# Kernel optimization log

Hardware: AMD Instinct MI355X
Metric: run time of the kernel (lower is better)

## Reference

```python
import jax, jax.numpy as jnp
import numpy as np

N_NODES = 50000
N_EDGES = 1600000
D_IN = 256
N_HEADS = 4
D_OUT = 32
NEG_SLOPE = 0.2


def setup_inputs() -> dict:
    key = jax.random.key(0)
    ks = jax.random.split(key, 7)
    return {
        "feat": jax.random.normal(ks[0], (N_NODES, D_IN), dtype=jnp.float32),
        "fc_w": jax.random.normal(ks[1], (N_HEADS * D_OUT, D_IN), dtype=jnp.float32) * 0.05,
        "attn_l": jax.random.normal(ks[2], (1, N_HEADS, D_OUT), dtype=jnp.float32) * 0.1,
        "attn_r": jax.random.normal(ks[3], (1, N_HEADS, D_OUT), dtype=jnp.float32) * 0.1,
        "bias": jax.random.normal(ks[4], (N_HEADS * D_OUT,), dtype=jnp.float32) * 0.01,
        "src": jax.random.randint(ks[5], (N_EDGES,), 0, N_NODES, dtype=jnp.int32),
        "dst": jax.random.randint(ks[6], (N_EDGES,), 0, N_NODES, dtype=jnp.int32),
    }


def reference(feat, fc_w, attn_l, attn_r, bias, src, dst):
    N = feat.shape[0]
    H, D = attn_l.shape[1], attn_l.shape[2]
    # projected features: [N, H, D] (torch Linear: x @ W.T)
    h = (feat @ fc_w.T).reshape(N, H, D)
    # per-node attention logits: [N, H]
    el = (h * attn_l).sum(-1)
    er = (h * attn_r).sum(-1)
    # per-edge score with leaky relu: [E, H]
    e = el[src] + er[dst]
    e = jnp.where(e > 0, e, NEG_SLOPE * e)
    # edge softmax normalized over incoming edges of each dst node
    m = jax.ops.segment_max(e, dst, num_segments=N)
    m = jnp.where(jnp.isfinite(m), m, 0.0)  # nodes with no in-edges
    ex = jnp.exp(e - m[dst])
    denom = jax.ops.segment_sum(ex, dst, num_segments=N)
    a = ex / jnp.maximum(denom[dst], 1e-9)  # [E, H]
    # weighted scatter-aggregate: [N, H, D]
    msg = h[src] * a[:, :, None]
    out = jax.ops.segment_sum(msg, dst, num_segments=N)
    out = out + bias.reshape(1, H, D)
    return out
```

## Files before the change

### kernel.cpp

```cpp
#include <hip/hip_runtime.h>
#include <hip/hip_bf16.h>
#include <math.h>

#define D_IN   256
#define HD     128
#define NHEAD  4
#define NEG_SLOPE 0.2f
#define CHUNK 32
#define MAXB  1024
#define BCAP  2560

typedef _Float16 h8 __attribute__((ext_vector_type(8)));
typedef _Float16 h4 __attribute__((ext_vector_type(4)));
typedef _Float16 h2 __attribute__((ext_vector_type(2)));
typedef float f4 __attribute__((ext_vector_type(4)));

#define SWZ(row, byte) ((byte) ^ (((row) & 7) << 4))

__global__ void zero_k(int* __restrict__ gcur, int B) {
    int i = blockIdx.x * 256 + threadIdx.x;
    if (i < B) gcur[i] = 0;
}

__global__ __launch_bounds__(256) void bin_k(const int* __restrict__ src,
                                             const int* __restrict__ dst,
                                             int* __restrict__ gcur,
                                             unsigned int* __restrict__ pairs,
                                             int E, int B) {
    __shared__ int lcnt[MAXB];
    __shared__ int lbase[MAXB];
    const int t = threadIdx.x;
    for (int i = t; i < B; i += 256) lcnt[i] = 0;
    __syncthreads();
    const int base = blockIdx.x * 4096;
    int sv[16], dv[16];
    #pragma unroll
    for (int k = 0; k < 16; ++k) {
        int idx = base + k * 256 + t;
        if (idx < E) {
            sv[k] = src[idx];
            dv[k] = dst[idx];
            atomicAdd(&lcnt[dv[k] >> 6], 1);
        } else dv[k] = -1;
    }
    __syncthreads();
    for (int i = t; i < B; i += 256) {
        int c = lcnt[i];
        lbase[i] = c ? atomicAdd(&gcur[i], c) : 0;
        lcnt[i] = 0;
    }
    __syncthreads();
    #pragma unroll
    for (int k = 0; k < 16; ++k) {
        if (dv[k] >= 0) {
            int b = dv[k] >> 6;
            int r = lbase[b] + atomicAdd(&lcnt[b], 1);
            if (r < BCAP)
                pairs[(size_t)b * BCAP + r] = ((unsigned int)sv[k] << 6) | (unsigned int)(dv[k] & 63);
        }
    }
}

__global__ __launch_bounds__(256) void bucket_k(const unsigned int* __restrict__ pairs,
                                                const int* __restrict__ gcur,
                                                int* __restrict__ row_start,
                                                int* __restrict__ degs,
                                                int* __restrict__ srcs, int N) {
    __shared__ int cnt64[64];
    __shared__ int base64[64];
    const int b = blockIdx.x;
    const int t = threadIdx.x;
    const int lo = b * BCAP;
    const int len = min(gcur[b], BCAP);
    if (t < 64) cnt64[t] = 0;
    __syncthreads();
    for (int i = t; i < len; i += 256)
        atomicAdd(&cnt64[pairs[lo + i] & 63], 1);
    __syncthreads();
    if (t < 64) {
        int v = cnt64[t];
        int x = v;
        #pragma unroll
        for (int o = 1; o < 64; o <<= 1) {
            int y = __shfl_up(x, o);
            if (t >= o) x += y;
        }
        int excl = lo + x - v;
        base64[t] = excl;
        int d = b * 64 + t;
        if (d < N) { row_start[d] = excl; degs[d] = v; }
        cnt64[t] = 0;
    }
    __syncthreads();
    for (int i = lo + t; i < lo + len; i += 256) {
        unsigned int p = pairs[i];
        int ld = p & 63;
        int r = atomicAdd(&cnt64[ld], 1);
        srcs[base64[ld] + r] = (int)(p >> 6);
    }
}

__global__ __launch_bounds__(256) void gemm_k(
        const float* __restrict__ feat, const float* __restrict__ fcw,
        const float* __restrict__ attn_l, const float* __restrict__ attn_r,
        unsigned int* __restrict__ hbuf, float* __restrict__ el, float* __restrict__ er,
        int N) {
    __shared__ __align__(16) unsigned char lds_raw[64 * 512];
    const int t  = threadIdx.x;
    const int l  = t & 63;
    const int w  = t >> 6;
    const int l4 = l >> 4;
    const int lm = l & 15;
    const int n0 = blockIdx.x * 64;

    h8 breg[2][8];
    #pragma unroll
    for (int jt = 0; jt < 2; ++jt) {
        const float* wrow = fcw + (size_t)(w * 32 + jt * 16 + lm) * D_IN;
        #pragma unroll
        for (int ks = 0; ks < 8; ++ks) {
            int k = ks * 32 + l4 * 8;
            float4 a = *(const float4*)&wrow[k];
            float4 b = *(const float4*)&wrow[k + 4];
            h8 p = {(_Float16)a.x, (_Float16)a.y, (_Float16)a.z, (_Float16)a.w,
                    (_Float16)b.x, (_Float16)b.y, (_Float16)b.z, (_Float16)b.w};
            breg[jt][ks] = p;
        }
    }

    #pragma unroll
    for (int i = 0; i < 16; ++i) {
        int idx = t + 256 * i;
        int row = idx >> 6, c4 = idx & 63;
        float4 v = make_float4(0.f, 0.f, 0.f, 0.f);
        if (n0 + row < N) v = *(const float4*)&feat[(size_t)(n0 + row) * D_IN + c4 * 4];
        h4 p = {(_Float16)v.x, (_Float16)v.y, (_Float16)v.z, (_Float16)v.w};
        *(h4*)(lds_raw + row * 512 + SWZ(row, c4 * 8)) = p;
    }
    __syncthreads();

    f4 acc[4][2] = {};
    #pragma unroll
    for (int ks = 0; ks < 8; ++ks) {
        #pragma unroll
        for (int mt = 0; mt < 4; ++mt) {
            int row = mt * 16 + lm;
            h8 af = *(const h8*)(lds_raw + row * 512 + SWZ(row, (ks * 32 + l4 * 8) * 2));
            acc[mt][0] = __builtin_amdgcn_mfma_f32_16x16x32_f16(af, breg[0][ks], acc[mt][0], 0, 0, 0);
            acc[mt][1] = __builtin_amdgcn_mfma_f32_16x16x32_f16(af, breg[1][ks], acc[mt][1], 0, 0, 0);
        }
    }

    float al[2], ar[2];
    #pragma unroll
    for (int jt = 0; jt < 2; ++jt) {
        al[jt] = attn_l[w * 32 + jt * 16 + lm];
        ar[jt] = attn_r[w * 32 + jt * 16 + lm];
    }
    #pragma unroll
    for (int mt = 0; mt < 4; ++mt) {
        #pragma unroll
        for (int r = 0; r < 4; ++r) {
            float vl = acc[mt][0][r] * al[0] + acc[mt][1][r] * al[1];
            float vr = acc[mt][0][r] * ar[0] + acc[mt][1][r] * ar[1];
            #pragma unroll
            for (int o = 1; o < 16; o <<= 1) {
                vl += __shfl_xor(vl, o);
                vr += __shfl_xor(vr, o);
            }
            int node = n0 + mt * 16 + l4 * 4 + r;
            if (lm == 0 && node < N) {
                el[node * NHEAD + w] = vl;
                er[node * NHEAD + w] = vr;
            }
        }
    }

    __syncthreads();
    unsigned short* hl = (unsigned short*)lds_raw;
    #pragma unroll
    for (int mt = 0; mt < 4; ++mt)
        #pragma unroll
        for (int jt = 0; jt < 2; ++jt)
            #pragma unroll
            for (int r = 0; r < 4; ++r) {
                int node_local = mt * 16 + l4 * 4 + r;
                int ch = w * 32 + jt * 16 + lm;
                _Float16 hf = (_Float16)acc[mt][jt][r];
                hl[node_local * 128 + ch] = __builtin_bit_cast(unsigned short, hf);
            }
    __syncthreads();
    const unsigned int* hu = (const unsigned int*)lds_raw;
    #pragma unroll
    for (int i = 0; i < 16; ++i) {
        int idx = t + 256 * i;
        int row = idx >> 6, c = idx & 63;
        if (n0 + row < N) hbuf[(size_t)(n0 + row) * 64 + c] = hu[row * 64 + c];
    }
}

__global__ __launch_bounds__(64) void agg_k(
        const int* __restrict__ row_start, const int* __restrict__ degs,
        const int* __restrict__ srcs,
        const float* __restrict__ el, const float* __restrict__ er,
        const unsigned int* __restrict__ hbuf, const float* __restrict__ bias,
        float* __restrict__ out, int N) {
    __shared__ float exw[CHUNK * NHEAD];
    __shared__ int s_lds[CHUNK];
    const int d = blockIdx.x;
    const int l = threadIdx.x;
    const int he = l >> 4, es = l & 15;
    const int half = l >> 5, cl = l & 31;
    const int hc = cl >> 3;
    const int base = row_start[d];
    const int deg  = degs[d];
    const float erd = er[d * NHEAD + he];

    f4 acc = {0.f, 0.f, 0.f, 0.f};
    float den = 0.f;

    for (int c0 = 0; c0 < deg; c0 += CHUNK) {
        const int clen = min(CHUNK, deg - c0);
        __syncthreads();
        int s0 = -1, s1 = -1;
        if (es < clen)      s0 = srcs[base + c0 + es];
        if (es + 16 < clen) s1 = srcs[base + c0 + es + 16];
        float e0 = 0.f, e1 = 0.f;
        if (s0 >= 0) e0 = el[s0 * NHEAD + he];
        if (s1 >= 0) e1 = el[s1 * NHEAD + he];
        if (s0 >= 0) {
            float v = e0 + erd;
            v = v > 0.f ? v : NEG_SLOPE * v;
            float ex = __expf(v);
            if (he == 0) s_lds[es] = s0;
            exw[es * NHEAD + he] = ex;
            den += ex;
        }
        if (s1 >= 0) {
            float v = e1 + erd;
            v = v > 0.f ? v : NEG_SLOPE * v;
            float ex = __expf(v);
            if (he == 0) s_lds[es + 16] = s1;
            exw[(es + 16) * NHEAD + he] = ex;
            den += ex;
        }
        __syncthreads();
        for (int jj = 0; jj < clen; jj += 8) {
            uint2 hv[4];
            float ex4[4];
            int e2v[4];
            #pragma unroll
            for (int k = 0; k < 4; ++k) {
                int e2 = jj + 2 * k + half;
                e2v[k] = (e2 < clen) ? e2 : -1;
                if (e2v[k] >= 0) {
                    int s = s_lds[e2];
                    hv[k] = *(const uint2*)&hbuf[(size_t)s * 64 + cl * 2];
                    ex4[k] = exw[e2 * NHEAD + hc];
                }
            }
            #pragma unroll
            for (int k = 0; k < 4; ++k) {
                if (e2v[k] >= 0) {
                    h2 p0 = __builtin_bit_cast(h2, hv[k].x);
                    h2 p1 = __builtin_bit_cast(h2, hv[k].y);
                    acc[0] += (float)p0[0] * ex4[k];
                    acc[1] += (float)p0[1] * ex4[k];
                    acc[2] += (float)p1[0] * ex4[k];
                    acc[3] += (float)p1[1] * ex4[k];
                }
            }
        }
    }

    #pragma unroll
    for (int k = 0; k < 4; ++k) acc[k] += __shfl_xor(acc[k], 32);
    #pragma unroll
    for (int o = 1; o < 16; o <<= 1) den += __shfl_xor(den, o);
    float denc = __shfl(den, hc << 4);
    float r = 1.0f / fmaxf(denc, 1e-9f);

    if (half == 0) {
        float4 b4 = *(const float4*)&bias[cl * 4];
        float4 o4 = make_float4(acc[0] * r + b4.x, acc[1] * r + b4.y,
                                acc[2] * r + b4.z, acc[3] * r + b4.w);
        *(float4*)&out[(size_t)d * HD + cl * 4] = o4;
    }
}

extern "C" void kernel_launch(void* const* d_in, const int* in_sizes, int n_in,
                              void* d_out, int out_size, void* d_ws, size_t ws_size,
                              hipStream_t stream) {
    const float* feat   = (const float*)d_in[0];
    const float* fcw    = (const float*)d_in[1];
    const float* attn_l = (const float*)d_in[2];
    const float* attn_r = (const float*)d_in[3];
    const float* bias   = (const float*)d_in[4];
    const int*   src    = (const int*)d_in[5];
    const int*   dst    = (const int*)d_in[6];
    float* out = (float*)d_out;

    const int N = in_sizes[0] / D_IN;
    const int E = in_sizes[5];
    const int B = (N + 63) >> 6;

    unsigned int* hbuf = (unsigned int*)d_ws;
    float* el        = (float*)(hbuf + (size_t)N * 64);
    float* er        = el + (size_t)N * NHEAD;
    unsigned int* pairs = (unsigned int*)(er + (size_t)N * NHEAD);
    int*   srcs      = (int*)(pairs + (size_t)B * BCAP);
    int*   row_start = srcs + (size_t)B * BCAP;
    int*   degs      = row_start + N;
    int*   gcur      = degs + N;

    const int ebl = (E + 4095) / 4096;

    zero_k<<<(B + 255) / 256, 256, 0, stream>>>(gcur, B);
    bin_k<<<ebl, 256, 0, stream>>>(src, dst, gcur, pairs, E, B);
    bucket_k<<<B, 256, 0, stream>>>(pairs, gcur, row_start, degs, srcs, N);
    gemm_k<<<(N + 63) / 64, 256, 0, stream>>>(feat, fcw, attn_l, attn_r, hbuf, el, er, N);
    agg_k<<<N, 64, 0, stream>>>(row_start, degs, srcs, el, er, hbuf, bias, out, N);
}
```

Measured before the change: 137.9 us.

## Fuse GEMM with edge binning and restructure aggregation to wave-per-node

Merges the edge binning kernel and the projection GEMM into one launch, with block index selecting the role, so the two independent phases run concurrently. The zeroing kernel is replaced by a memset. The aggregation kernel now maps one wavefront per destination node, four nodes per block. It broadcasts source indices and exp weights through shuffles instead of LDS and barriers, and loads 16-byte feature vectors per lane. This removes per-node launch granularity and syncthreads overhead but adds shuffle work and extra cross-lane reductions.

```diff
diff --git a/kernel.cpp b/kernel.cpp
--- a/kernel.cpp
+++ b/kernel.cpp
@@ -6,7 +6,6 @@
 #define HD     128
 #define NHEAD  4
 #define NEG_SLOPE 0.2f
-#define CHUNK 32
 #define MAXB  1024
 #define BCAP  2560
 
@@ -17,47 +16,141 @@
 
 #define SWZ(row, byte) ((byte) ^ (((row) & 7) << 4))
 
-__global__ void zero_k(int* __restrict__ gcur, int B) {
-    int i = blockIdx.x * 256 + threadIdx.x;
-    if (i < B) gcur[i] = 0;
-}
-
-__global__ __launch_bounds__(256) void bin_k(const int* __restrict__ src,
-                                             const int* __restrict__ dst,
-                                             int* __restrict__ gcur,
-                                             unsigned int* __restrict__ pairs,
-                                             int E, int B) {
-    __shared__ int lcnt[MAXB];
-    __shared__ int lbase[MAXB];
+__global__ __launch_bounds__(256) void fused_k(
+        const float* __restrict__ feat, const float* __restrict__ fcw,
+        const float* __restrict__ attn_l, const float* __restrict__ attn_r,
+        unsigned int* __restrict__ hbuf, float* __restrict__ el, float* __restrict__ er,
+        const int* __restrict__ src, const int* __restrict__ dst,
+        int* __restrict__ gcur, unsigned int* __restrict__ pairs,
+        int N, int E, int B, int GB) {
+    __shared__ __align__(16) unsigned char smem[64 * 512];
     const int t = threadIdx.x;
-    for (int i = t; i < B; i += 256) lcnt[i] = 0;
-    __syncthreads();
-    const int base = blockIdx.x * 4096;
-    int sv[16], dv[16];
-    #pragma unroll
-    for (int k = 0; k < 16; ++k) {
-        int idx = base + k * 256 + t;
-        if (idx < E) {
-            sv[k] = src[idx];
-            dv[k] = dst[idx];
-            atomicAdd(&lcnt[dv[k] >> 6], 1);
-        } else dv[k] = -1;
-    }
-    __syncthreads();
-    for (int i = t; i < B; i += 256) {
-        int c = lcnt[i];
-        lbase[i] = c ? atomicAdd(&gcur[i], c) : 0;
-        lcnt[i] = 0;
-    }
-    __syncthreads();
-    #pragma unroll
-    for (int k = 0; k < 16; ++k) {
-        if (dv[k] >= 0) {
-            int b = dv[k] >> 6;
-            int r = lbase[b] + atomicAdd(&lcnt[b], 1);
-            if (r < BCAP)
-                pairs[(size_t)b * BCAP + r] = ((unsigned int)sv[k] << 6) | (unsigned int)(dv[k] & 63);
-        }
+
+    if ((int)blockIdx.x >= GB) {
+        int* lcnt  = (int*)smem;
+        int* lbase = lcnt + MAXB;
+        for (int i = t; i < B; i += 256) lcnt[i] = 0;
+        __syncthreads();
+        const int base = ((int)blockIdx.x - GB) * 4096;
+        int sv[16], dv[16];
+        #pragma unroll
+        for (int k = 0; k < 16; ++k) {
+            int idx = base + k * 256 + t;
+            if (idx < E) {
+                sv[k] = src[idx];
+                dv[k] = dst[idx];
+                atomicAdd(&lcnt[dv[k] >> 6], 1);
+            } else dv[k] = -1;
+        }
+        __syncthreads();
+        for (int i = t; i < B; i += 256) {
+            int c = lcnt[i];
+            lbase[i] = c ? atomicAdd(&gcur[i], c) : 0;
+            lcnt[i] = 0;
+        }
+        __syncthreads();
+        #pragma unroll
+        for (int k = 0; k < 16; ++k) {
+            if (dv[k] >= 0) {
+                int b = dv[k] >> 6;
+                int r = lbase[b] + atomicAdd(&lcnt[b], 1);
+                if (r < BCAP)
+                    pairs[(size_t)b * BCAP + r] = ((unsigned int)sv[k] << 6) | (unsigned int)(dv[k] & 63);
+            }
+        }
+        return;
+    }
+
+    unsigned char* lds_raw = smem;
+    const int l  = t & 63;
+    const int w  = t >> 6;
+    const int l4 = l >> 4;
+    const int lm = l & 15;
+    const int n0 = blockIdx.x * 64;
+
+    h8 breg[2][8];
+    #pragma unroll
+    for (int jt = 0; jt < 2; ++jt) {
+        const float* wrow = fcw + (size_t)(w * 32 + jt * 16 + lm) * D_IN;
+        #pragma unroll
+        for (int ks = 0; ks < 8; ++ks) {
+            int k = ks * 32 + l4 * 8;
+            float4 a = *(const float4*)&wrow[k];
+            float4 b = *(const float4*)&wrow[k + 4];
+            h8 p = {(_Float16)a.x, (_Float16)a.y, (_Float16)a.z, (_Float16)a.w,
+                    (_Float16)b.x, (_Float16)b.y, (_Float16)b.z, (_Float16)b.w};
+            breg[jt][ks] = p;
+        }
+    }
+
+    #pragma unroll
+    for (int i = 0; i < 16; ++i) {
+        int idx = t + 256 * i;
+        int row = idx >> 6, c4 = idx & 63;
+        float4 v = make_float4(0.f, 0.f, 0.f, 0.f);
+        if (n0 + row < N) v = *(const float4*)&feat[(size_t)(n0 + row) * D_IN + c4 * 4];
+        h4 p = {(_Float16)v.x, (_Float16)v.y, (_Float16)v.z, (_Float16)v.w};
+        *(h4*)(lds_raw + row * 512 + SWZ(row, c4 * 8)) = p;
+    }
+    __syncthreads();
+
+    f4 acc[4][2] = {};
+    #pragma unroll
+    for (int ks = 0; ks < 8; ++ks) {
+        #pragma unroll
+        for (int mt = 0; mt < 4; ++mt) {
+            int row = mt * 16 + lm;
+            h8 af = *(const h8*)(lds_raw + row * 512 + SWZ(row, (ks * 32 + l4 * 8) * 2));
+            acc[mt][0] = __builtin_amdgcn_mfma_f32_16x16x32_f16(af, breg[0][ks], acc[mt][0], 0, 0, 0);
+            acc[mt][1] = __builtin_amdgcn_mfma_f32_16x16x32_f16(af, breg[1][ks], acc[mt][1], 0, 0, 0);
+        }
+    }
+
+    float al[2], ar[2];
+    #pragma unroll
+    for (int jt = 0; jt < 2; ++jt) {
+        al[jt] = attn_l[w * 32 + jt * 16 + lm];
+        ar[jt] = attn_r[w * 32 + jt * 16 + lm];
+    }
+    #pragma unroll
+    for (int mt = 0; mt < 4; ++mt) {
+        #pragma unroll
+        for (int r = 0; r < 4; ++r) {
+            float vl = acc[mt][0][r] * al[0] + acc[mt][1][r] * al[1];
+            float vr = acc[mt][0][r] * ar[0] + acc[mt][1][r] * ar[1];
+            #pragma unroll
+            for (int o = 1; o < 16; o <<= 1) {
+                vl += __shfl_xor(vl, o);
+                vr += __shfl_xor(vr, o);
+            }
+            int node = n0 + mt * 16 + l4 * 4 + r;
+            if (lm == 0 && node < N) {
+                el[node * NHEAD + w] = vl;
+                er[node * NHEAD + w] = vr;
+            }
+        }
+    }
+
+    __syncthreads();
+    unsigned short* hl = (unsigned short*)lds_raw;
+    #pragma unroll
+    for (int mt = 0; mt < 4; ++mt)
+        #pragma unroll
+        for (int jt = 0; jt < 2; ++jt)
+            #pragma unroll
+            for (int r = 0; r < 4; ++r) {
+                int node_local = mt * 16 + l4 * 4 + r;
+                int ch = w * 32 + jt * 16 + lm;
+                _Float16 hf = (_Float16)acc[mt][jt][r];
+                hl[node_local * 128 + ch] = __builtin_bit_cast(unsigned short, hf);
+            }
+    __syncthreads();
+    const unsigned int* hu = (const unsigned int*)lds_raw;
+    #pragma unroll
+    for (int i = 0; i < 16; ++i) {
+        int idx = t + 256 * i;
+        int row = idx >> 6, c = idx & 63;
+        if (n0 + row < N) hbuf[(size_t)(n0 + row) * 64 + c] = hu[row * 64 + c];
     }
 }
 
@@ -100,191 +193,90 @@
     }
 }
 
-__global__ __launch_bounds__(256) void gemm_k(
-        const float* __restrict__ feat, const float* __restrict__ fcw,
-        const float* __restrict__ attn_l, const float* __restrict__ attn_r,
-        unsigned int* __restrict__ hbuf, float* __restrict__ el, float* __restrict__ er,
-        int N) {
-    __shared__ __align__(16) unsigned char lds_raw[64 * 512];
-    const int t  = threadIdx.x;
-    const int l  = t & 63;
-    const int w  = t >> 6;
-    const int l4 = l >> 4;
-    const int lm = l & 15;
-    const int n0 = blockIdx.x * 64;
-
-    h8 breg[2][8];
-    #pragma unroll
-    for (int jt = 0; jt < 2; ++jt) {
-        const float* wrow = fcw + (size_t)(w * 32 + jt * 16 + lm) * D_IN;
-        #pragma unroll
-        for (int ks = 0; ks < 8; ++ks) {
-            int k = ks * 32 + l4 * 8;
-            float4 a = *(const float4*)&wrow[k];
-            float4 b = *(const float4*)&wrow[k + 4];
-            h8 p = {(_Float16)a.x, (_Float16)a.y, (_Float16)a.z, (_Float16)a.w,
-                    (_Float16)b.x, (_Float16)b.y, (_Float16)b.z, (_Float16)b.w};
-            breg[jt][ks] = p;
-        }
-    }
-
-    #pragma unroll
-    for (int i = 0; i < 16; ++i) {
-        int idx = t + 256 * i;
-        int row = idx >> 6, c4 = idx & 63;
-        float4 v = make_float4(0.f, 0.f, 0.f, 0.f);
-        if (n0 + row < N) v = *(const float4*)&feat[(size_t)(n0 + row) * D_IN + c4 * 4];
-        h4 p = {(_Float16)v.x, (_Float16)v.y, (_Float16)v.z, (_Float16)v.w};
-        *(h4*)(lds_raw + row * 512 + SWZ(row, c4 * 8)) = p;
-    }
-    __syncthreads();
-
-    f4 acc[4][2] = {};
-    #pragma unroll
-    for (int ks = 0; ks < 8; ++ks) {
-        #pragma unroll
-        for (int mt = 0; mt < 4; ++mt) {
-            int row = mt * 16 + lm;
-            h8 af = *(const h8*)(lds_raw + row * 512 + SWZ(row, (ks * 32 + l4 * 8) * 2));
-            acc[mt][0] = __builtin_amdgcn_mfma_f32_16x16x32_f16(af, breg[0][ks], acc[mt][0], 0, 0, 0);
-            acc[mt][1] = __builtin_amdgcn_mfma_f32_16x16x32_f16(af, breg[1][ks], acc[mt][1], 0, 0, 0);
-        }
-    }
-
-    float al[2], ar[2];
-    #pragma unroll
-    for (int jt = 0; jt < 2; ++jt) {
-        al[jt] = attn_l[w * 32 + jt * 16 + lm];
-        ar[jt] = attn_r[w * 32 + jt * 16 + lm];
-    }
-    #pragma unroll
-    for (int mt = 0; mt < 4; ++mt) {
-        #pragma unroll
-        for (int r = 0; r < 4; ++r) {
-            float vl = acc[mt][0][r] * al[0] + acc[mt][1][r] * al[1];
-            float vr = acc[mt][0][r] * ar[0] + acc[mt][1][r] * ar[1];
-            #pragma unroll
-            for (int o = 1; o < 16; o <<= 1) {
-                vl += __shfl_xor(vl, o);
-                vr += __shfl_xor(vr, o);
-            }
-            int node = n0 + mt * 16 + l4 * 4 + r;
-            if (lm == 0 && node < N) {
-                el[node * NHEAD + w] = vl;
-                er[node * NHEAD + w] = vr;
-            }
-        }
-    }
-
-    __syncthreads();
-    unsigned short* hl = (unsigned short*)lds_raw;
-    #pragma unroll
-    for (int mt = 0; mt < 4; ++mt)
-        #pragma unroll
-        for (int jt = 0; jt < 2; ++jt)
-            #pragma unroll
-            for (int r = 0; r < 4; ++r) {
-                int node_local = mt * 16 + l4 * 4 + r;
-                int ch = w * 32 + jt * 16 + lm;
-                _Float16 hf = (_Float16)acc[mt][jt][r];
-                hl[node_local * 128 + ch] = __builtin_bit_cast(unsigned short, hf);
-            }
-    __syncthreads();
-    const unsigned int* hu = (const unsigned int*)lds_raw;
-    #pragma unroll
-    for (int i = 0; i < 16; ++i) {
-        int idx = t + 256 * i;
-        int row = idx >> 6, c = idx & 63;
-        if (n0 + row < N) hbuf[(size_t)(n0 + row) * 64 + c] = hu[row * 64 + c];
-    }
-}
-
-__global__ __launch_bounds__(64) void agg_k(
+__global__ __launch_bounds__(256) void agg_k(
         const int* __restrict__ row_start, const int* __restrict__ degs,
         const int* __restrict__ srcs,
         const float* __restrict__ el, const float* __restrict__ er,
         const unsigned int* __restrict__ hbuf, const float* __restrict__ bias,
         float* __restrict__ out, int N) {
-    __shared__ float exw[CHUNK * NHEAD];
-    __shared__ int s_lds[CHUNK];
-    const int d = blockIdx.x;
-    const int l = threadIdx.x;
-    const int he = l >> 4, es = l & 15;
-    const int half = l >> 5, cl = l & 31;
-    const int hc = cl >> 3;
+    const int l = threadIdx.x & 63;
+    const int d = blockIdx.x * 4 + (threadIdx.x >> 6);
+    if (d >= N) return;
+    const int q  = l >> 4;
+    const int es = l & 15;
+    const int hc = es >> 2;
     const int base = row_start[d];
     const int deg  = degs[d];
-    const float erd = er[d * NHEAD + he];
-
-    f4 acc = {0.f, 0.f, 0.f, 0.f};
+    const float erd = er[d * NHEAD + q];
+
+    float acc[8] = {0.f, 0.f, 0.f, 0.f, 0.f, 0.f, 0.f, 0.f};
     float den = 0.f;
 
-    for (int c0 = 0; c0 < deg; c0 += CHUNK) {
-        const int clen = min(CHUNK, deg - c0);
-        __syncthreads();
-        int s0 = -1, s1 = -1;
-        if (es < clen)      s0 = srcs[base + c0 + es];
-        if (es + 16 < clen) s1 = srcs[base + c0 + es + 16];
-        float e0 = 0.f, e1 = 0.f;
-        if (s0 >= 0) e0 = el[s0 * NHEAD + he];
-        if (s1 >= 0) e1 = el[s1 * NHEAD + he];
-        if (s0 >= 0) {
-            float v = e0 + erd;
+    for (int c0 = 0; c0 < deg; c0 += 32) {
+        const int clen = min(32, deg - c0);
+        int s0 = 0, s1 = 0;
+        float ex0 = 0.f, ex1 = 0.f;
+        if (es < clen) {
+            s0 = srcs[base + c0 + es];
+            float v = el[s0 * NHEAD + q] + erd;
             v = v > 0.f ? v : NEG_SLOPE * v;
-            float ex = __expf(v);
-            if (he == 0) s_lds[es] = s0;
-            exw[es * NHEAD + he] = ex;
-            den += ex;
-        }
-        if (s1 >= 0) {
-            float v = e1 + erd;
+            ex0 = __expf(v);
+            den += ex0;
+        }
+        if (es + 16 < clen) {
+            s1 = srcs[base + c0 + es + 16];
+            float v = el[s1 * NHEAD + q] + erd;
             v = v > 0.f ? v : NEG_SLOPE * v;
-            float ex = __expf(v);
-            if (he == 0) s_lds[es + 16] = s1;
-            exw[(es + 16) * NHEAD + he] = ex;
-            den += ex;
-        }
-        __syncthreads();
-        for (int jj = 0; jj < clen; jj += 8) {
-            uint2 hv[4];
-            float ex4[4];
-            int e2v[4];
+            ex1 = __expf(v);
+            den += ex1;
+        }
+        for (int jj = 0; jj < clen; jj += 16) {
+            uint4 hv[4];
+            float exv[4];
             #pragma unroll
             for (int k = 0; k < 4; ++k) {
-                int e2 = jj + 2 * k + half;
-                e2v[k] = (e2 < clen) ? e2 : -1;
-                if (e2v[k] >= 0) {
-                    int s = s_lds[e2];
-                    hv[k] = *(const uint2*)&hbuf[(size_t)s * 64 + cl * 2];
-                    ex4[k] = exw[e2 * NHEAD + hc];
-                }
+                int e4 = jj + k * 4 + q;
+                int ls = e4 & 15;
+                int sa = __shfl(s0, ls);
+                int sb = __shfl(s1, ls);
+                float ea = __shfl(ex0, hc * 16 + ls);
+                float eb = __shfl(ex1, hc * 16 + ls);
+                int s = (e4 < 16) ? sa : sb;
+                exv[k] = (e4 < clen) ? ((e4 < 16) ? ea : eb) : 0.f;
+                hv[k] = *(const uint4*)&hbuf[(size_t)s * 64 + es * 4];
             }
             #pragma unroll
             for (int k = 0; k < 4; ++k) {
-                if (e2v[k] >= 0) {
-                    h2 p0 = __builtin_bit_cast(h2, hv[k].x);
-                    h2 p1 = __builtin_bit_cast(h2, hv[k].y);
-                    acc[0] += (float)p0[0] * ex4[k];
-                    acc[1] += (float)p0[1] * ex4[k];
-                    acc[2] += (float)p1[0] * ex4[k];
-                    acc[3] += (float)p1[1] * ex4[k];
+                #pragma unroll
+                for (int c = 0; c < 4; ++c) {
+                    unsigned int u = (&hv[k].x)[c];
+                    h2 p = __builtin_bit_cast(h2, u);
+                    acc[2 * c]     += (float)p[0] * exv[k];
+                    acc[2 * c + 1] += (float)p[1] * exv[k];
                 }
             }
         }
     }
 
     #pragma unroll
-    for (int k = 0; k < 4; ++k) acc[k] += __shfl_xor(acc[k], 32);
+    for (int c = 0; c < 8; ++c) {
+        acc[c] += __shfl_xor(acc[c], 16);
+        acc[c] += __shfl_xor(acc[c], 32);
+    }
     #pragma unroll
     for (int o = 1; o < 16; o <<= 1) den += __shfl_xor(den, o);
     float denc = __shfl(den, hc << 4);
-    float r = 1.0f / fmaxf(denc, 1e-9f);
-
-    if (half == 0) {
-        float4 b4 = *(const float4*)&bias[cl * 4];
-        float4 o4 = make_float4(acc[0] * r + b4.x, acc[1] * r + b4.y,
-                                acc[2] * r + b4.z, acc[3] * r + b4.w);
-        *(float4*)&out[(size_t)d * HD + cl * 4] = o4;
+
+    if (q == 0) {
+        float r = 1.0f / fmaxf(denc, 1e-9f);
+        float4 b0 = *(const float4*)&bias[es * 8];
+        float4 b1 = *(const float4*)&bias[es * 8 + 4];
+        float4 o0 = make_float4(acc[0] * r + b0.x, acc[1] * r + b0.y,
+                                acc[2] * r + b0.z, acc[3] * r + b0.w);
+        float4 o1 = make_float4(acc[4] * r + b1.x, acc[5] * r + b1.y,
+                                acc[6] * r + b1.z, acc[7] * r + b1.w);
+        *(float4*)&out[(size_t)d * HD + es * 8]     = o0;
+        *(float4*)&out[(size_t)d * HD + es * 8 + 4] = o1;
     }
 }
 
@@ -313,11 +305,12 @@
     int*   degs      = row_start + N;
     int*   gcur      = degs + N;
 
+    const int GB  = (N + 63) / 64;
     const int ebl = (E + 4095) / 4096;
 
-    zero_k<<<(B + 255) / 256, 256, 0, stream>>>(gcur, B);
-    bin_k<<<ebl, 256, 0, stream>>>(src, dst, gcur, pairs, E, B);
+    hipMemsetAsync(gcur, 0, (size_t)B * sizeof(int), stream);
+    fused_k<<<GB + ebl, 256, 0, stream>>>(feat, fcw, attn_l, attn_r, hbuf, el, er,
+                                          src, dst, gcur, pairs, N, E, B, GB);
     bucket_k<<<B, 256, 0, stream>>>(pairs, gcur, row_start, degs, srcs, N);
-    gemm_k<<<(N + 63) / 64, 256, 0, stream>>>(feat, fcw, attn_l, attn_r, hbuf, el, er, N);
-    agg_k<<<N, 64, 0, stream>>>(row_start, degs, srcs, el, er, hbuf, bias, out, N);
+    agg_k<<<(N + 3) / 4, 256, 0, stream>>>(row_start, degs, srcs, el, er, hbuf, bias, out, N);
 }
```

Measured after the change: 131.7 us. -4.5%, faster.

## Fuse edge binning and projection GEMM into one launch, pre-convert weights

Applied to the files above, without the earlier changes.

Merges the edge-binning kernel and the feature-projection GEMM kernel into a single launch whose blocks split by index. Blocks below GB run the GEMM and the rest bin edges, so the two independent stages overlap on the GPU. The fc weight is converted to fp16 once by a small kernel, so GEMM blocks no longer each convert fp32 weights. The zero kernel becomes a hipMemsetAsync. The fused kernel's register and LDS use is the maximum of the two paths, which may lower occupancy for the lighter binning blocks.

```diff
diff --git a/kernel.cpp b/kernel.cpp
--- a/kernel.cpp
+++ b/kernel.cpp
@@ -17,47 +17,144 @@
 
 #define SWZ(row, byte) ((byte) ^ (((row) & 7) << 4))
 
-__global__ void zero_k(int* __restrict__ gcur, int B) {
+__global__ __launch_bounds__(256) void wconv_k(const float* __restrict__ fcw,
+                                               unsigned short* __restrict__ wf16) {
     int i = blockIdx.x * 256 + threadIdx.x;
-    if (i < B) gcur[i] = 0;
-}
-
-__global__ __launch_bounds__(256) void bin_k(const int* __restrict__ src,
-                                             const int* __restrict__ dst,
-                                             int* __restrict__ gcur,
-                                             unsigned int* __restrict__ pairs,
-                                             int E, int B) {
-    __shared__ int lcnt[MAXB];
-    __shared__ int lbase[MAXB];
+    float4 v = *(const float4*)&fcw[i * 4];
+    h4 p = {(_Float16)v.x, (_Float16)v.y, (_Float16)v.z, (_Float16)v.w};
+    *(h4*)&wf16[i * 4] = p;
+}
+
+__global__ __launch_bounds__(256) void fused_k(
+        const float* __restrict__ feat, const unsigned short* __restrict__ wf16,
+        const float* __restrict__ attn_l, const float* __restrict__ attn_r,
+        unsigned int* __restrict__ hbuf, float* __restrict__ el, float* __restrict__ er,
+        const int* __restrict__ src, const int* __restrict__ dst,
+        int* __restrict__ gcur, unsigned int* __restrict__ pairs,
+        int N, int E, int B, int GB) {
+    __shared__ __align__(16) unsigned char smem[64 * 512];
     const int t = threadIdx.x;
-    for (int i = t; i < B; i += 256) lcnt[i] = 0;
-    __syncthreads();
-    const int base = blockIdx.x * 4096;
-    int sv[16], dv[16];
-    #pragma unroll
-    for (int k = 0; k < 16; ++k) {
-        int idx = base + k * 256 + t;
-        if (idx < E) {
-            sv[k] = src[idx];
-            dv[k] = dst[idx];
-            atomicAdd(&lcnt[dv[k] >> 6], 1);
-        } else dv[k] = -1;
-    }
-    __syncthreads();
-    for (int i = t; i < B; i += 256) {
-        int c = lcnt[i];
-        lbase[i] = c ? atomicAdd(&gcur[i], c) : 0;
-        lcnt[i] = 0;
-    }
-    __syncthreads();
-    #pragma unroll
-    for (int k = 0; k < 16; ++k) {
-        if (dv[k] >= 0) {
-            int b = dv[k] >> 6;
-            int r = lbase[b] + atomicAdd(&lcnt[b], 1);
-            if (r < BCAP)
-                pairs[(size_t)b * BCAP + r] = ((unsigned int)sv[k] << 6) | (unsigned int)(dv[k] & 63);
-        }
+
+    if ((int)blockIdx.x >= GB) {
+        int* lcnt  = (int*)smem;
+        int* lbase = lcnt + MAXB;
+        for (int i = t; i < B; i += 256) lcnt[i] = 0;
+        __syncthreads();
+        const int base = ((int)blockIdx.x - GB) * 4096;
+        int sv[16], dv[16];
+        #pragma unroll
+        for (int k = 0; k < 16; ++k) {
+            int idx = base + k * 256 + t;
+            if (idx < E) {
+                sv[k] = src[idx];
+                dv[k] = dst[idx];
+                atomicAdd(&lcnt[dv[k] >> 6], 1);
+            } else dv[k] = -1;
+        }
+        __syncthreads();
+        for (int i = t; i < B; i += 256) {
+            int c = lcnt[i];
+            lbase[i] = c ? atomicAdd(&gcur[i], c) : 0;
+            lcnt[i] = 0;
+        }
+        __syncthreads();
+        #pragma unroll
+        for (int k = 0; k < 16; ++k) {
+            if (dv[k] >= 0) {
+                int b = dv[k] >> 6;
+                int r = lbase[b] + atomicAdd(&lcnt[b], 1);
+                if (r < BCAP)
+                    pairs[(size_t)b * BCAP + r] =
+                        ((unsigned int)sv[k] << 6) | (unsigned int)(dv[k] & 63);
+            }
+        }
+        return;
+    }
+
+    unsigned char* lds_raw = smem;
+    const int l  = t & 63;
+    const int w  = t >> 6;
+    const int l4 = l >> 4;
+    const int lm = l & 15;
+    const int n0 = blockIdx.x * 64;
+
+    h8 breg[2][8];
+    #pragma unroll
+    for (int jt = 0; jt < 2; ++jt) {
+        const unsigned short* wrow = wf16 + (size_t)(w * 32 + jt * 16 + lm) * D_IN;
+        #pragma unroll
+        for (int ks = 0; ks < 8; ++ks)
+            breg[jt][ks] = *(const h8*)&wrow[ks * 32 + l4 * 8];
+    }
+
+    #pragma unroll
+    for (int i = 0; i < 16; ++i) {
+        int idx = t + 256 * i;
+        int row = idx >> 6, c4 = idx & 63;
+        float4 v = make_float4(0.f, 0.f, 0.f, 0.f);
+        if (n0 + row < N) v = *(const float4*)&feat[(size_t)(n0 + row) * D_IN + c4 * 4];
+        h4 p = {(_Float16)v.x, (_Float16)v.y, (_Float16)v.z, (_Float16)v.w};
+        *(h4*)(lds_raw + row * 512 + SWZ(row, c4 * 8)) = p;
+    }
+    __syncthreads();
+
+    f4 acc[4][2] = {};
+    #pragma unroll
+    for (int ks = 0; ks < 8; ++ks) {
+        #pragma unroll
+        for (int mt = 0; mt < 4; ++mt) {
+            int row = mt * 16 + lm;
+            h8 af = *(const h8*)(lds_raw + row * 512 + SWZ(row, (ks * 32 + l4 * 8) * 2));
+            acc[mt][0] = __builtin_amdgcn_mfma_f32_16x16x32_f16(af, breg[0][ks], acc[mt][0], 0, 0, 0);
+            acc[mt][1] = __builtin_amdgcn_mfma_f32_16x16x32_f16(af, breg[1][ks], acc[mt][1], 0, 0, 0);
+        }
+    }
+
+    float al[2], ar[2];
+    #pragma unroll
+    for (int jt = 0; jt < 2; ++jt) {
+        al[jt] = attn_l[w * 32 + jt * 16 + lm];
+        ar[jt] = attn_r[w * 32 + jt * 16 + lm];
+    }
+    #pragma unroll
+    for (int mt = 0; mt < 4; ++mt) {
+        #pragma unroll
+        for (int r = 0; r < 4; ++r) {
+            float vl = acc[mt][0][r] * al[0] + acc[mt][1][r] * al[1];
+            float vr = acc[mt][0][r] * ar[0] + acc[mt][1][r] * ar[1];
+            #pragma unroll
+            for (int o = 1; o < 16; o <<= 1) {
+                vl += __shfl_xor(vl, o);
+                vr += __shfl_xor(vr, o);
+            }
+            int node = n0 + mt * 16 + l4 * 4 + r;
+            if (lm == 0 && node < N) {
+                el[node * NHEAD + w] = vl;
+                er[node * NHEAD + w] = vr;
+            }
+        }
+    }
+
+    __syncthreads();
+    unsigned short* hl = (unsigned short*)lds_raw;
+    #pragma unroll
+    for (int mt = 0; mt < 4; ++mt)
+        #pragma unroll
+        for (int jt = 0; jt < 2; ++jt)
+            #pragma unroll
+            for (int r = 0; r < 4; ++r) {
+                int node_local = mt * 16 + l4 * 4 + r;
+                int ch = w * 32 + jt * 16 + lm;
+                _Float16 hf = (_Float16)acc[mt][jt][r];
+                hl[node_local * 128 + ch] = __builtin_bit_cast(unsigned short, hf);
+            }
+    __syncthreads();
+    const unsigned int* hu = (const unsigned int*)lds_raw;
+    #pragma unroll
+    for (int i = 0; i < 16; ++i) {
+        int idx = t + 256 * i;
+        int row = idx >> 6, c = idx & 63;
+        if (n0 + row < N) hbuf[(size_t)(n0 + row) * 64 + c] = hu[row * 64 + c];
     }
 }
 
@@ -97,105 +194,6 @@
         int ld = p & 63;
         int r = atomicAdd(&cnt64[ld], 1);
         srcs[base64[ld] + r] = (int)(p >> 6);
-    }
-}
-
-__global__ __launch_bounds__(256) void gemm_k(
-        const float* __restrict__ feat, const float* __restrict__ fcw,
-        const float* __restrict__ attn_l, const float* __restrict__ attn_r,
-        unsigned int* __restrict__ hbuf, float* __restrict__ el, float* __restrict__ er,
-        int N) {
-    __shared__ __align__(16) unsigned char lds_raw[64 * 512];
-    const int t  = threadIdx.x;
-    const int l  = t & 63;
-    const int w  = t >> 6;
-    const int l4 = l >> 4;
-    const int lm = l & 15;
-    const int n0 = blockIdx.x * 64;
-
-    h8 breg[2][8];
-    #pragma unroll
-    for (int jt = 0; jt < 2; ++jt) {
-        const float* wrow = fcw + (size_t)(w * 32 + jt * 16 + lm) * D_IN;
-        #pragma unroll
-        for (int ks = 0; ks < 8; ++ks) {
-            int k = ks * 32 + l4 * 8;
-            float4 a = *(const float4*)&wrow[k];
-            float4 b = *(const float4*)&wrow[k + 4];
-            h8 p = {(_Float16)a.x, (_Float16)a.y, (_Float16)a.z, (_Float16)a.w,
-                    (_Float16)b.x, (_Float16)b.y, (_Float16)b.z, (_Float16)b.w};
-            breg[jt][ks] = p;
-        }
-    }
-
-    #pragma unroll
-    for (int i = 0; i < 16; ++i) {
-        int idx = t + 256 * i;
-        int row = idx >> 6, c4 = idx & 63;
-        float4 v = make_float4(0.f, 0.f, 0.f, 0.f);
-        if (n0 + row < N) v = *(const float4*)&feat[(size_t)(n0 + row) * D_IN + c4 * 4];
-        h4 p = {(_Float16)v.x, (_Float16)v.y, (_Float16)v.z, (_Float16)v.w};
-        *(h4*)(lds_raw + row * 512 + SWZ(row, c4 * 8)) = p;
-    }
-    __syncthreads();
-
-    f4 acc[4][2] = {};
-    #pragma unroll
-    for (int ks = 0; ks < 8; ++ks) {
-        #pragma unroll
-        for (int mt = 0; mt < 4; ++mt) {
-            int row = mt * 16 + lm;
-            h8 af = *(const h8*)(lds_raw + row * 512 + SWZ(row, (ks * 32 + l4 * 8) * 2));
-            acc[mt][0] = __builtin_amdgcn_mfma_f32_16x16x32_f16(af, breg[0][ks], acc[mt][0], 0, 0, 0);
-            acc[mt][1] = __builtin_amdgcn_mfma_f32_16x16x32_f16(af, breg[1][ks], acc[mt][1], 0, 0, 0);
-        }
-    }
-
-    float al[2], ar[2];
-    #pragma unroll
-    for (int jt = 0; jt < 2; ++jt) {
-        al[jt] = attn_l[w * 32 + jt * 16 + lm];
-        ar[jt] = attn_r[w * 32 + jt * 16 + lm];
-    }
-    #pragma unroll
-    for (int mt = 0; mt < 4; ++mt) {
-        #pragma unroll
-        for (int r = 0; r < 4; ++r) {
-            float vl = acc[mt][0][r] * al[0] + acc[mt][1][r] * al[1];
-            float vr = acc[mt][0][r] * ar[0] + acc[mt][1][r] * ar[1];
-            #pragma unroll
-            for (int o = 1; o < 16; o <<= 1) {
-                vl += __shfl_xor(vl, o);
-                vr += __shfl_xor(vr, o);
-            }
-            int node = n0 + mt * 16 + l4 * 4 + r;
-            if (lm == 0 && node < N) {
-                el[node * NHEAD + w] = vl;
-                er[node * NHEAD + w] = vr;
-            }
-        }
-    }
-
-    __syncthreads();
-    unsigned short* hl = (unsigned short*)lds_raw;
-    #pragma unroll
-    for (int mt = 0; mt < 4; ++mt)
-        #pragma unroll
-        for (int jt = 0; jt < 2; ++jt)
-            #pragma unroll
-            for (int r = 0; r < 4; ++r) {
-                int node_local = mt * 16 + l4 * 4 + r;
-                int ch = w * 32 + jt * 16 + lm;
-                _Float16 hf = (_Float16)acc[mt][jt][r];
-                hl[node_local * 128 + ch] = __builtin_bit_cast(unsigned short, hf);
-            }
-    __syncthreads();
-    const unsigned int* hu = (const unsigned int*)lds_raw;
-    #pragma unroll
-    for (int i = 0; i < 16; ++i) {
-        int idx = t + 256 * i;
-        int row = idx >> 6, c = idx & 63;
-        if (n0 + row < N) hbuf[(size_t)(n0 + row) * 64 + c] = hu[row * 64 + c];
     }
 }
 
@@ -307,17 +305,20 @@
     unsigned int* hbuf = (unsigned int*)d_ws;
     float* el        = (float*)(hbuf + (size_t)N * 64);
     float* er        = el + (size_t)N * NHEAD;
-    unsigned int* pairs = (unsigned int*)(er + (size_t)N * NHEAD);
+    unsigned short* wf16 = (unsigned short*)(er + (size_t)N * NHEAD);
+    unsigned int* pairs = (unsigned int*)(wf16 + HD * D_IN);
     int*   srcs      = (int*)(pairs + (size_t)B * BCAP);
     int*   row_start = srcs + (size_t)B * BCAP;
     int*   degs      = row_start + N;
     int*   gcur      = degs + N;
 
+    const int GB  = (N + 63) / 64;
     const int ebl = (E + 4095) / 4096;
 
-    zero_k<<<(B + 255) / 256, 256, 0, stream>>>(gcur, B);
-    bin_k<<<ebl, 256, 0, stream>>>(src, dst, gcur, pairs, E, B);
+    hipMemsetAsync(gcur, 0, (size_t)B * sizeof(int), stream);
+    wconv_k<<<(HD * D_IN / 4 + 255) / 256, 256, 0, stream>>>(fcw, wf16);
+    fused_k<<<GB + ebl, 256, 0, stream>>>(feat, wf16, attn_l, attn_r, hbuf, el, er,
+                                          src, dst, gcur, pairs, N, E, B, GB);
     bucket_k<<<B, 256, 0, stream>>>(pairs, gcur, row_start, degs, srcs, N);
-    gemm_k<<<(N + 63) / 64, 256, 0, stream>>>(feat, fcw, attn_l, attn_r, hbuf, el, er, N);
     agg_k<<<N, 64, 0, stream>>>(row_start, degs, srcs, el, er, hbuf, bias, out, N);
 }
```

Result: faster. 122.2 us (-11.3%).
